# Performance work log

Hardware: AMD Instinct MI355X
Metric: run time of the kernel (lower is better)

## Reference

```python
import jax, jax.numpy as jnp
import numpy as np

MEX_C = 2.0 / (np.sqrt(3.0) * np.pi ** 0.25)

def mexican_hat(z):
    return MEX_C * (z * z - 1.0) * jnp.exp(-0.5 * z * z)

def setup_inputs() -> dict:
    key = jax.random.key(0)
    ks = jax.random.split(key, 5)
    B, T, D, O = 4, 2048, 128, 128
    x = jax.random.normal(ks[0], (B, T, D), dtype=jnp.float32)
    # init like torch: scale ~ U(0.5,1.5), translation ~ U(-0.5,0.5), kaiming-ish weights
    scale = jax.random.uniform(ks[1], (O, D), dtype=jnp.float32, minval=0.5, maxval=1.5)
    translation = jax.random.uniform(ks[2], (O, D), dtype=jnp.float32, minval=-0.5, maxval=0.5)
    bound = 1.0 / np.sqrt(D)
    wavelet_weights = jax.random.uniform(ks[3], (O, D), dtype=jnp.float32, minval=-bound, maxval=bound)
    base_w = jax.random.uniform(ks[4], (O, D), dtype=jnp.float32, minval=-bound, maxval=bound)
    ln_gamma = jnp.ones((D,), dtype=jnp.float32)
    ln_beta = jnp.zeros((D,), dtype=jnp.float32)
    return {"x": x, "scale": scale, "translation": translation,
            "wavelet_weights": wavelet_weights, "base_w": base_w,
            "ln_gamma": ln_gamma, "ln_beta": ln_beta}

def reference(x, scale, translation, wavelet_weights, base_w, ln_gamma, ln_beta):
    B, T, D = x.shape
    O = wavelet_weights.shape[0]
    # LayerNorm over last dim (eps = 1e-5, torch default)
    mu = jnp.mean(x, axis=-1, keepdims=True)
    var = jnp.mean((x - mu) ** 2, axis=-1, keepdims=True)
    x_norm = (x - mu) / jnp.sqrt(var + 1e-5) * ln_gamma + ln_beta
    x_flat = x_norm.reshape(B * T, D)                      # (N, D)
    s = jax.nn.softplus(scale) + 0.1                       # (O, D)
    # broadcast intermediate (N, O, D) — the memory-bound path
    z = (x_flat[:, None, :] - translation[None]) / s[None]
    w = jnp.clip(mexican_hat(z), -10.0, 10.0)              # (N, O, D)
    wavelet_out = jnp.einsum('nod,od->no', w, wavelet_weights)
    base_out = x.reshape(B * T, D) @ base_w.T              # base uses raw x
    out = wavelet_out + jax.nn.silu(base_out)
    return out.reshape(B, T, O)
```

## Files before the change

### kernel.cpp

```cpp
#include <hip/hip_runtime.h>


#define D_DIM 128
#define O_DIM 128
#define ROWS  32
#define BLOCK 512
#define OH    64

#define C1     0.72134752f
#define SQRT_C 0.84932180f
#define WWK    1.2023651f
#define LOG2E  1.44269504f

typedef float v2f __attribute__((ext_vector_type(2)));

__device__ __forceinline__ unsigned bf16r(float f) {
    unsigned u = __float_as_uint(f);
    return (u + 0x7fffu + ((u >> 16) & 1u)) >> 16;
}

__device__ __forceinline__ v2f pk_fma_xhi_nlo(v2f x, v2f w) {
    v2f d;
    asm("v_pk_fma_f32 %0, %1, %2, %2 op_sel:[0,1,0] op_sel_hi:[1,1,0] neg_lo:[0,0,1] neg_hi:[0,0,1]"
        : "=v"(d) : "v"(x), "v"(w));
    return d;
}
__device__ __forceinline__ v2f pk_mul(v2f a, v2f b) {
    v2f d;
    asm("v_pk_mul_f32 %0, %1, %2" : "=v"(d) : "v"(a), "v"(b));
    return d;
}
__device__ __forceinline__ v2f pk_fma_lolo(v2f q, v2f w, v2f c) {
    v2f d;
    asm("v_pk_fma_f32 %0, %1, %2, %3 op_sel:[0,0,0] op_sel_hi:[1,0,0]"
        : "=v"(d) : "v"(q), "v"(w), "v"(c));
    return d;
}
__device__ __forceinline__ void pk_fma_vv(v2f& acc, v2f a, v2f b) {
    asm("v_pk_fma_f32 %0, %1, %2, %0" : "+v"(acc) : "v"(a), "v"(b));
}
__device__ __forceinline__ void pk_fma_acc_hi(v2f& acc, v2f s, v2f w) {
    asm("v_pk_fma_f32 %0, %1, %2, %0 op_sel:[0,1,0] op_sel_hi:[1,1,1]"
        : "+v"(acc) : "v"(s), "v"(w));
}

__global__ __launch_bounds__(256) void wavekan_prep(
    const float* __restrict__ scale,
    const float* __restrict__ trans,
    const float* __restrict__ ww,
    const float* __restrict__ bw,
    const float* __restrict__ gamma,
    uint2* __restrict__ wsW)
{
    int idx = blockIdx.x * blockDim.x + threadIdx.x;
    if (idx >= O_DIM * D_DIM) return;
    int o = idx >> 7;
    int d = idx & (D_DIM - 1);
    float sc = scale[idx];
    float sp = fmaxf(sc, 0.0f) + log1pf(__expf(-fabsf(sc)));
    float is2 = SQRT_C / (sp + 0.1f);
    float bwg = bw[idx] / gamma[d];
    uint2 w;
    w.x = bf16r(trans[idx] * is2) | (bf16r(is2) << 16);
    w.y = bf16r(ww[idx] * WWK)    | (bf16r(bwg) << 16);
    wsW[d * O_DIM + o] = w;
}

__global__ __launch_bounds__(128) void wavekan_prep2(
    const float* __restrict__ bw,
    const float* __restrict__ gamma,
    const float* __restrict__ beta,
    float2* __restrict__ cbsb)
{
    int o = blockIdx.x, t = threadIdx.x;
    float b  = bw[o * D_DIM + t];
    float bg = b / gamma[t];
    float cb = beta[t] * bg;
    float sb = b;
    #pragma unroll
    for (int m = 1; m < 64; m <<= 1) {
        cb += __shfl_xor(cb, m, 64);
        sb += __shfl_xor(sb, m, 64);
    }
    __shared__ float2 tmp[2];
    if ((t & 63) == 0) tmp[t >> 6] = make_float2(cb, sb);
    __syncthreads();
    if (t == 0) cbsb[o] = make_float2(tmp[0].x + tmp[1].x, tmp[0].y + tmp[1].y);
}

__global__ __launch_bounds__(BLOCK, 4) void wavekan_main(
    const float* __restrict__ x,
    const uint2* __restrict__ wsW,
    const float2* __restrict__ cbsb,
    const float* __restrict__ gamma,
    const float* __restrict__ beta,
    float* __restrict__ out,
    int N)
{
    __shared__ uint4  s_w4[D_DIM * OH / 2];
    __shared__ uint2  s_ln2[8 * D_DIM];
    __shared__ float2 s_mr[ROWS];

    const int tid  = threadIdx.x;
    const int h    = blockIdx.x & 1;
    const int row0 = (blockIdx.x >> 1) * ROWS;

    const uint4* wsW4 = reinterpret_cast<const uint4*>(wsW);
    #pragma unroll
    for (int k = 0; k < 8; ++k) {
        int flat = tid + k * BLOCK;
        int d = flat >> 5, z = flat & 31;
        s_w4[flat] = wsW4[d * 64 + h * 32 + z];
    }

    {
        const int r  = tid >> 4;
        const int j  = tid & 15;
        const int d0 = j * 8;
        const int grow = row0 + r;

        float v[8];
        if (grow < N) {
            const float4* p = reinterpret_cast<const float4*>(x + (size_t)grow * D_DIM + d0);
            float4 a = p[0], b4 = p[1];
            v[0]=a.x; v[1]=a.y; v[2]=a.z; v[3]=a.w;
            v[4]=b4.x; v[5]=b4.y; v[6]=b4.z; v[7]=b4.w;
        } else {
            #pragma unroll
            for (int k = 0; k < 8; ++k) v[k] = 0.0f;
        }
        float sum = 0.f, ssq = 0.f;
        #pragma unroll
        for (int k = 0; k < 8; ++k) { sum += v[k]; ssq += v[k] * v[k]; }
        #pragma unroll
        for (int m = 1; m < 16; m <<= 1) {
            sum += __shfl_xor(sum, m, 64);
            ssq += __shfl_xor(ssq, m, 64);
        }
        const float mean = sum * (1.0f / D_DIM);
        const float var  = ssq * (1.0f / D_DIM) - mean * mean;
        const float rstd = rsqrtf(var + 1e-5f);
        const float sv   = (var + 1e-5f) * rstd;

        const float4* pg = reinterpret_cast<const float4*>(gamma + d0);
        const float4* pb = reinterpret_cast<const float4*>(beta + d0);
        float4 g0 = pg[0], g1 = pg[1], b0 = pb[0], b1 = pb[1];
        float gg[8] = {g0.x,g0.y,g0.z,g0.w,g1.x,g1.y,g1.z,g1.w};
        float bb[8] = {b0.x,b0.y,b0.z,b0.w,b1.x,b1.y,b1.z,b1.w};

        const int gi  = r >> 2;
        const int sub = r & 3;
        unsigned short* sl = reinterpret_cast<unsigned short*>(s_ln2);
        #pragma unroll
        for (int k = 0; k < 8; ++k) {
            float ln = (v[k] - mean) * rstd * gg[k] + bb[k];
            sl[(gi * D_DIM + d0 + k) * 4 + sub] = (unsigned short)bf16r(ln);
        }
        if (j == 0) s_mr[r] = make_float2(mean, sv);
    }
    __syncthreads();

    const int lane = tid & 63;
    const int g    = tid >> 6;
    const int o    = h * OH + lane;
    const uint2* __restrict__ sw = reinterpret_cast<const uint2*>(s_w4);

    v2f accw01 = {0.f,0.f}, accw23 = {0.f,0.f};
    v2f accb01 = {0.f,0.f}, accb23 = {0.f,0.f};
    const v2f vNegC1 = {-C1, -C1};

    #pragma unroll 4
    for (int d = 0; d < D_DIM; ++d) {
        uint2 wv = sw[d * OH + lane];
        uint2 xv = s_ln2[g * D_DIM + d];
        v2f w01, w23, xln01, xln23;
        w01.x   = __uint_as_float(wv.x << 16);
        w01.y   = __uint_as_float(wv.x & 0xffff0000u);
        w23.x   = __uint_as_float(wv.y << 16);
        w23.y   = __uint_as_float(wv.y & 0xffff0000u);
        xln01.x = __uint_as_float(xv.x << 16);
        xln01.y = __uint_as_float(xv.x & 0xffff0000u);
        xln23.x = __uint_as_float(xv.y << 16);
        xln23.y = __uint_as_float(xv.y & 0xffff0000u);

        v2f wc  = pk_mul(w23, vNegC1);
        v2f u01 = pk_fma_xhi_nlo(xln01, w01);
        v2f u23 = pk_fma_xhi_nlo(xln23, w01);
        v2f q01 = pk_mul(u01, u01);
        v2f q23 = pk_mul(u23, u23);
        v2f e01 = {__builtin_amdgcn_exp2f(-q01.x), __builtin_amdgcn_exp2f(-q01.y)};
        v2f e23 = {__builtin_amdgcn_exp2f(-q23.x), __builtin_amdgcn_exp2f(-q23.y)};
        v2f p01 = pk_fma_lolo(q01, w23, wc);
        v2f p23 = pk_fma_lolo(q23, w23, wc);
        pk_fma_vv(accw01, p01, e01);
        pk_fma_vv(accw23, p23, e23);
        pk_fma_acc_hi(accb01, xln01, w23);
        pk_fma_acc_hi(accb23, xln23, w23);
    }

    float2 cs = cbsb[o];
    float aw[4] = {accw01.x, accw01.y, accw23.x, accw23.y};
    float ab[4] = {accb01.x, accb01.y, accb23.x, accb23.y};
    #pragma unroll
    for (int k = 0; k < 4; ++k) {
        const int rr = row0 + g * 4 + k;
        if (rr < N) {
            float2 mr  = s_mr[g * 4 + k];
            float base = (ab[k] - cs.x) * mr.y + mr.x * cs.y;
            float sig  = 1.0f / (1.0f + __builtin_amdgcn_exp2f(-LOG2E * base));
            out[(size_t)rr * O_DIM + o] = aw[k] + base * sig;
        }
    }
}

__global__ __launch_bounds__(1024, 8) void wavekan_main_fb(
    const float* __restrict__ x,
    const float* __restrict__ scale,
    const float* __restrict__ trans,
    const float* __restrict__ ww,
    const float* __restrict__ bw,
    const float* __restrict__ gamma,
    const float* __restrict__ beta,
    float* __restrict__ out,
    int N)
{
    __shared__ float4 s_x[128 * 9];
    const int tid = threadIdx.x;
    const int row0 = blockIdx.x * 16;
    {
        const int r = tid >> 6, j = tid & 63, d0 = j * 2;
        const int grow = row0 + r;
        float2 v2 = make_float2(0.f, 0.f);
        if (grow < N) v2 = *reinterpret_cast<const float2*>(x + (size_t)grow * D_DIM + d0);
        float sum = v2.x + v2.y, ssq = v2.x * v2.x + v2.y * v2.y;
        #pragma unroll
        for (int m = 1; m < 64; m <<= 1) { sum += __shfl_xor(sum, m, 64); ssq += __shfl_xor(ssq, m, 64); }
        const float mean = sum / 128.f, var = ssq / 128.f - mean * mean;
        const float rstd = rsqrtf(var + 1e-5f);
        float2 g2 = *reinterpret_cast<const float2*>(gamma + d0);
        float2 b2 = *reinterpret_cast<const float2*>(beta + d0);
        const int p = r >> 1, hh = r & 1;
        float* c0 = reinterpret_cast<float*>(&s_x[d0 * 9 + p]);
        float* c1 = reinterpret_cast<float*>(&s_x[(d0 + 1) * 9 + p]);
        c0[hh] = (v2.x - mean) * rstd * g2.x + b2.x; c0[2 + hh] = v2.x;
        c1[hh] = (v2.y - mean) * rstd * g2.y + b2.y; c1[2 + hh] = v2.y;
    }
    __syncthreads();
    const int o = tid & 127, g = tid >> 7;
    float aw0 = 0.f, aw1 = 0.f, ab0 = 0.f, ab1 = 0.f;
    for (int d = 0; d < D_DIM; ++d) {
        int idx = o * D_DIM + d;
        float sc = scale[idx];
        float sp = fmaxf(sc, 0.0f) + log1pf(__expf(-fabsf(sc)));
        float is = SQRT_C / (sp + 0.1f);
        float tws = trans[idx] * is, wwk = ww[idx] * WWK, bwv = bw[idx];
        float4 xx = s_x[d * 9 + g];
        float u0 = fmaf(xx.x, is, -tws), u1 = fmaf(xx.y, is, -tws);
        float q0 = u0 * u0, q1 = u1 * u1;
        aw0 = fmaf((q0 - C1) * __builtin_amdgcn_exp2f(-q0), wwk, aw0);
        aw1 = fmaf((q1 - C1) * __builtin_amdgcn_exp2f(-q1), wwk, aw1);
        ab0 = fmaf(xx.z, bwv, ab0);
        ab1 = fmaf(xx.w, bwv, ab1);
    }
    const int rr0 = row0 + g * 2;
    if (rr0 < N) {
        float s0 = 1.0f / (1.0f + __builtin_amdgcn_exp2f(-LOG2E * ab0));
        out[(size_t)rr0 * O_DIM + o] = aw0 + ab0 * s0;
    }
    if (rr0 + 1 < N) {
        float s1 = 1.0f / (1.0f + __builtin_amdgcn_exp2f(-LOG2E * ab1));
        out[(size_t)(rr0 + 1) * O_DIM + o] = aw1 + ab1 * s1;
    }
}

extern "C" void kernel_launch(void* const* d_in, const int* in_sizes, int n_in,
                              void* d_out, int out_size, void* d_ws, size_t ws_size,
                              hipStream_t stream) {
    const float* x     = (const float*)d_in[0];
    const float* scale = (const float*)d_in[1];
    const float* trans = (const float*)d_in[2];
    const float* ww    = (const float*)d_in[3];
    const float* bw    = (const float*)d_in[4];
    const float* gamma = (const float*)d_in[5];
    const float* beta  = (const float*)d_in[6];
    float* out = (float*)d_out;

    const int N = in_sizes[0] / D_DIM;

    const size_t tbl_bytes = (size_t)O_DIM * D_DIM * sizeof(uint2);
    const size_t ws_needed = tbl_bytes + O_DIM * sizeof(float2);
    if (ws_size >= ws_needed) {
        uint2*  tbl  = (uint2*)d_ws;
        float2* cbsb = (float2*)((char*)d_ws + tbl_bytes);
        wavekan_prep<<<(O_DIM * D_DIM + 255) / 256, 256, 0, stream>>>(
            scale, trans, ww, bw, gamma, tbl);
        wavekan_prep2<<<O_DIM, 128, 0, stream>>>(bw, gamma, beta, cbsb);
        const int grid = ((N + ROWS - 1) / ROWS) * 2;
        wavekan_main<<<grid, BLOCK, 0, stream>>>(
            x, tbl, cbsb, gamma, beta, out, N);
    } else {
        wavekan_main_fb<<<(N + 15) / 16, 1024, 0, stream>>>(
            x, scale, trans, ww, bw, gamma, beta, out, N);
    }
}
```

Before: 101.9 us.

## Split outputs into quarters, fold beta into translation, drop packed-math asm

Each block now covers a quarter of the outputs (32 columns) for 32 rows, so every thread computes 2 rows × 1 output instead of 4 rows × 1. The LDS weight tile shrinks, which allows launch bounds of 8 waves per SIMD. LayerNorm beta is folded into the precomputed translation term, and the base correction is simplified so it no longer needs the beta-dependent sum or the per-row mean/std smem table. The hand-written v_pk_fma inline asm is replaced with scalar fmaf. The risks are losing packed FP32 throughput, recomputing LayerNorm four times per row group instead of twice, and more weight tile loads overall.

Result: slower. 106.8 us (+4.9%).

```diff
diff --git a/kernel.cpp b/kernel.cpp
--- a/kernel.cpp
+++ b/kernel.cpp
@@ -5,43 +5,16 @@
 #define O_DIM 128
 #define ROWS  32
 #define BLOCK 512
-#define OH    64
+#define OQ    32
 
 #define C1     0.72134752f
 #define SQRT_C 0.84932180f
 #define WWK    1.2023651f
 #define LOG2E  1.44269504f
 
-typedef float v2f __attribute__((ext_vector_type(2)));
-
 __device__ __forceinline__ unsigned bf16r(float f) {
     unsigned u = __float_as_uint(f);
     return (u + 0x7fffu + ((u >> 16) & 1u)) >> 16;
-}
-
-__device__ __forceinline__ v2f pk_fma_xhi_nlo(v2f x, v2f w) {
-    v2f d;
-    asm("v_pk_fma_f32 %0, %1, %2, %2 op_sel:[0,1,0] op_sel_hi:[1,1,0] neg_lo:[0,0,1] neg_hi:[0,0,1]"
-        : "=v"(d) : "v"(x), "v"(w));
-    return d;
-}
-__device__ __forceinline__ v2f pk_mul(v2f a, v2f b) {
-    v2f d;
-    asm("v_pk_mul_f32 %0, %1, %2" : "=v"(d) : "v"(a), "v"(b));
-    return d;
-}
-__device__ __forceinline__ v2f pk_fma_lolo(v2f q, v2f w, v2f c) {
-    v2f d;
-    asm("v_pk_fma_f32 %0, %1, %2, %3 op_sel:[0,0,0] op_sel_hi:[1,0,0]"
-        : "=v"(d) : "v"(q), "v"(w), "v"(c));
-    return d;
-}
-__device__ __forceinline__ void pk_fma_vv(v2f& acc, v2f a, v2f b) {
-    asm("v_pk_fma_f32 %0, %1, %2, %0" : "+v"(acc) : "v"(a), "v"(b));
-}
-__device__ __forceinline__ void pk_fma_acc_hi(v2f& acc, v2f s, v2f w) {
-    asm("v_pk_fma_f32 %0, %1, %2, %0 op_sel:[0,1,0] op_sel_hi:[1,1,1]"
-        : "+v"(acc) : "v"(s), "v"(w));
 }
 
 __global__ __launch_bounds__(256) void wavekan_prep(
@@ -50,6 +23,7 @@
     const float* __restrict__ ww,
     const float* __restrict__ bw,
     const float* __restrict__ gamma,
+    const float* __restrict__ beta,
     uint2* __restrict__ wsW)
 {
     int idx = blockIdx.x * blockDim.x + threadIdx.x;
@@ -59,60 +33,55 @@
     float sc = scale[idx];
     float sp = fmaxf(sc, 0.0f) + log1pf(__expf(-fabsf(sc)));
     float is2 = SQRT_C / (sp + 0.1f);
+    float tis2 = (beta[d] - trans[idx]) * is2;
     float bwg = bw[idx] / gamma[d];
     uint2 w;
-    w.x = bf16r(trans[idx] * is2) | (bf16r(is2) << 16);
-    w.y = bf16r(ww[idx] * WWK)    | (bf16r(bwg) << 16);
+    w.x = bf16r(tis2)          | (bf16r(is2) << 16);
+    w.y = bf16r(ww[idx] * WWK) | (bf16r(bwg) << 16);
     wsW[d * O_DIM + o] = w;
 }
 
 __global__ __launch_bounds__(128) void wavekan_prep2(
     const float* __restrict__ bw,
-    const float* __restrict__ gamma,
-    const float* __restrict__ beta,
-    float2* __restrict__ cbsb)
+    float* __restrict__ sb)
 {
     int o = blockIdx.x, t = threadIdx.x;
-    float b  = bw[o * D_DIM + t];
-    float bg = b / gamma[t];
-    float cb = beta[t] * bg;
-    float sb = b;
+    float s = bw[o * D_DIM + t];
     #pragma unroll
-    for (int m = 1; m < 64; m <<= 1) {
-        cb += __shfl_xor(cb, m, 64);
-        sb += __shfl_xor(sb, m, 64);
-    }
-    __shared__ float2 tmp[2];
-    if ((t & 63) == 0) tmp[t >> 6] = make_float2(cb, sb);
+    for (int m = 1; m < 64; m <<= 1) s += __shfl_xor(s, m, 64);
+    __shared__ float tmp[2];
+    if ((t & 63) == 0) tmp[t >> 6] = s;
     __syncthreads();
-    if (t == 0) cbsb[o] = make_float2(tmp[0].x + tmp[1].x, tmp[0].y + tmp[1].y);
-}
-
-__global__ __launch_bounds__(BLOCK, 4) void wavekan_main(
+    if (t == 0) sb[o] = tmp[0] + tmp[1];
+}
+
+__global__ __launch_bounds__(BLOCK, 8) void wavekan_main(
     const float* __restrict__ x,
     const uint2* __restrict__ wsW,
-    const float2* __restrict__ cbsb,
+    const float* __restrict__ sb,
     const float* __restrict__ gamma,
-    const float* __restrict__ beta,
     float* __restrict__ out,
     int N)
 {
-    __shared__ uint4  s_w4[D_DIM * OH / 2];
-    __shared__ uint2  s_ln2[8 * D_DIM];
-    __shared__ float2 s_mr[ROWS];
+    __shared__ uint2 s_w[D_DIM * OQ];
+    __shared__ unsigned s_ln[16 * D_DIM];
 
     const int tid  = threadIdx.x;
-    const int h    = blockIdx.x & 1;
-    const int row0 = (blockIdx.x >> 1) * ROWS;
-
-    const uint4* wsW4 = reinterpret_cast<const uint4*>(wsW);
-    #pragma unroll
-    for (int k = 0; k < 8; ++k) {
-        int flat = tid + k * BLOCK;
-        int d = flat >> 5, z = flat & 31;
-        s_w4[flat] = wsW4[d * 64 + h * 32 + z];
-    }
-
+    const int q    = blockIdx.x & 3;
+    const int row0 = (blockIdx.x >> 2) * ROWS;
+
+    {
+        const uint4* wsW4 = reinterpret_cast<const uint4*>(wsW);
+        uint4* sw4 = reinterpret_cast<uint4*>(s_w);
+        #pragma unroll
+        for (int k = 0; k < 4; ++k) {
+            int flat = tid + k * BLOCK;
+            int d = flat >> 4, i = flat & 15;
+            sw4[flat] = wsW4[d * 64 + q * 16 + i];
+        }
+    }
+
+    float mean, sv;
     {
         const int r  = tid >> 4;
         const int j  = tid & 15;
@@ -137,78 +106,76 @@
             sum += __shfl_xor(sum, m, 64);
             ssq += __shfl_xor(ssq, m, 64);
         }
-        const float mean = sum * (1.0f / D_DIM);
+        mean = sum * (1.0f / D_DIM);
         const float var  = ssq * (1.0f / D_DIM) - mean * mean;
         const float rstd = rsqrtf(var + 1e-5f);
-        const float sv   = (var + 1e-5f) * rstd;
+        sv = (var + 1e-5f) * rstd;
 
         const float4* pg = reinterpret_cast<const float4*>(gamma + d0);
-        const float4* pb = reinterpret_cast<const float4*>(beta + d0);
-        float4 g0 = pg[0], g1 = pg[1], b0 = pb[0], b1 = pb[1];
+        float4 g0 = pg[0], g1 = pg[1];
         float gg[8] = {g0.x,g0.y,g0.z,g0.w,g1.x,g1.y,g1.z,g1.w};
-        float bb[8] = {b0.x,b0.y,b0.z,b0.w,b1.x,b1.y,b1.z,b1.w};
-
-        const int gi  = r >> 2;
-        const int sub = r & 3;
-        unsigned short* sl = reinterpret_cast<unsigned short*>(s_ln2);
+
+        unsigned short* sl = reinterpret_cast<unsigned short*>(s_ln);
+        const int pr  = r >> 1;
+        const int hlf = r & 1;
         #pragma unroll
         for (int k = 0; k < 8; ++k) {
-            float ln = (v[k] - mean) * rstd * gg[k] + bb[k];
-            sl[(gi * D_DIM + d0 + k) * 4 + sub] = (unsigned short)bf16r(ln);
-        }
-        if (j == 0) s_mr[r] = make_float2(mean, sv);
+            float ln = (v[k] - mean) * rstd * gg[k];
+            sl[(pr * D_DIM + d0 + k) * 2 + hlf] = (unsigned short)bf16r(ln);
+        }
     }
     __syncthreads();
 
     const int lane = tid & 63;
     const int g    = tid >> 6;
-    const int o    = h * OH + lane;
-    const uint2* __restrict__ sw = reinterpret_cast<const uint2*>(s_w4);
-
-    v2f accw01 = {0.f,0.f}, accw23 = {0.f,0.f};
-    v2f accb01 = {0.f,0.f}, accb23 = {0.f,0.f};
-    const v2f vNegC1 = {-C1, -C1};
+    const int ol   = lane & 31;
+    const int ph   = lane >> 5;
+    const int kpr  = 2 * g + ph;
+
+    float accw0 = 0.f, accw1 = 0.f, accb0 = 0.f, accb1 = 0.f;
 
     #pragma unroll 4
     for (int d = 0; d < D_DIM; ++d) {
-        uint2 wv = sw[d * OH + lane];
-        uint2 xv = s_ln2[g * D_DIM + d];
-        v2f w01, w23, xln01, xln23;
-        w01.x   = __uint_as_float(wv.x << 16);
-        w01.y   = __uint_as_float(wv.x & 0xffff0000u);
-        w23.x   = __uint_as_float(wv.y << 16);
-        w23.y   = __uint_as_float(wv.y & 0xffff0000u);
-        xln01.x = __uint_as_float(xv.x << 16);
-        xln01.y = __uint_as_float(xv.x & 0xffff0000u);
-        xln23.x = __uint_as_float(xv.y << 16);
-        xln23.y = __uint_as_float(xv.y & 0xffff0000u);
-
-        v2f wc  = pk_mul(w23, vNegC1);
-        v2f u01 = pk_fma_xhi_nlo(xln01, w01);
-        v2f u23 = pk_fma_xhi_nlo(xln23, w01);
-        v2f q01 = pk_mul(u01, u01);
-        v2f q23 = pk_mul(u23, u23);
-        v2f e01 = {__builtin_amdgcn_exp2f(-q01.x), __builtin_amdgcn_exp2f(-q01.y)};
-        v2f e23 = {__builtin_amdgcn_exp2f(-q23.x), __builtin_amdgcn_exp2f(-q23.y)};
-        v2f p01 = pk_fma_lolo(q01, w23, wc);
-        v2f p23 = pk_fma_lolo(q23, w23, wc);
-        pk_fma_vv(accw01, p01, e01);
-        pk_fma_vv(accw23, p23, e23);
-        pk_fma_acc_hi(accb01, xln01, w23);
-        pk_fma_acc_hi(accb23, xln23, w23);
-    }
-
-    float2 cs = cbsb[o];
-    float aw[4] = {accw01.x, accw01.y, accw23.x, accw23.y};
-    float ab[4] = {accb01.x, accb01.y, accb23.x, accb23.y};
-    #pragma unroll
-    for (int k = 0; k < 4; ++k) {
-        const int rr = row0 + g * 4 + k;
-        if (rr < N) {
-            float2 mr  = s_mr[g * 4 + k];
-            float base = (ab[k] - cs.x) * mr.y + mr.x * cs.y;
+        uint2 wv    = s_w[d * OQ + ol];
+        unsigned xv = s_ln[kpr * D_DIM + d];
+        float tis = __uint_as_float(wv.x << 16);
+        float isv = __uint_as_float(wv.x & 0xffff0000u);
+        float wwk = __uint_as_float(wv.y << 16);
+        float bwg = __uint_as_float(wv.y & 0xffff0000u);
+        float x0  = __uint_as_float(xv << 16);
+        float x1  = __uint_as_float(xv & 0xffff0000u);
+
+        float u0 = fmaf(x0, isv, tis);
+        float u1 = fmaf(x1, isv, tis);
+        float q0 = u0 * u0, q1 = u1 * u1;
+        float e0 = __builtin_amdgcn_exp2f(-q0);
+        float e1 = __builtin_amdgcn_exp2f(-q1);
+        float wc = wwk * (-C1);
+        float p0 = fmaf(q0, wwk, wc);
+        float p1 = fmaf(q1, wwk, wc);
+        accw0 = fmaf(p0, e0, accw0);
+        accw1 = fmaf(p1, e1, accw1);
+        accb0 = fmaf(x0, bwg, accb0);
+        accb1 = fmaf(x1, bwg, accb1);
+    }
+
+    {
+        const int og  = q * OQ + ol;
+        const float sbv = sb[og];
+        float m0 = __shfl(mean, ph * 32,      64);
+        float s0 = __shfl(sv,   ph * 32,      64);
+        float m1 = __shfl(mean, ph * 32 + 16, 64);
+        float s1 = __shfl(sv,   ph * 32 + 16, 64);
+        const int r0 = row0 + 4 * g + 2 * ph;
+        if (r0 < N) {
+            float base = fmaf(s0, accb0, m0 * sbv);
             float sig  = 1.0f / (1.0f + __builtin_amdgcn_exp2f(-LOG2E * base));
-            out[(size_t)rr * O_DIM + o] = aw[k] + base * sig;
+            out[(size_t)r0 * O_DIM + og] = accw0 + base * sig;
+        }
+        if (r0 + 1 < N) {
+            float base = fmaf(s1, accb1, m1 * sbv);
+            float sig  = 1.0f / (1.0f + __builtin_amdgcn_exp2f(-LOG2E * base));
+            out[(size_t)(r0 + 1) * O_DIM + og] = accw1 + base * sig;
         }
     }
 }
@@ -288,16 +255,16 @@
     const int N = in_sizes[0] / D_DIM;
 
     const size_t tbl_bytes = (size_t)O_DIM * D_DIM * sizeof(uint2);
-    const size_t ws_needed = tbl_bytes + O_DIM * sizeof(float2);
+    const size_t ws_needed = tbl_bytes + O_DIM * sizeof(float);
     if (ws_size >= ws_needed) {
-        uint2*  tbl  = (uint2*)d_ws;
-        float2* cbsb = (float2*)((char*)d_ws + tbl_bytes);
+        uint2* tbl = (uint2*)d_ws;
+        float* sbp = (float*)((char*)d_ws + tbl_bytes);
         wavekan_prep<<<(O_DIM * D_DIM + 255) / 256, 256, 0, stream>>>(
-            scale, trans, ww, bw, gamma, tbl);
-        wavekan_prep2<<<O_DIM, 128, 0, stream>>>(bw, gamma, beta, cbsb);
-        const int grid = ((N + ROWS - 1) / ROWS) * 2;
+            scale, trans, ww, bw, gamma, beta, tbl);
+        wavekan_prep2<<<O_DIM, 128, 0, stream>>>(bw, sbp);
+        const int grid = ((N + ROWS - 1) / ROWS) * 4;
         wavekan_main<<<grid, BLOCK, 0, stream>>>(
-            x, tbl, cbsb, gamma, beta, out, N);
+            x, tbl, sbp, gamma, out, N);
     } else {
         wavekan_main_fb<<<(N + 15) / 16, 1024, 0, stream>>>(
             x, scale, trans, ww, bw, gamma, beta, out, N);
```
